# Kernel optimization log

Measured on AMD Instinct MI355X. Metric: run time of the kernel, lower is better.

The kernel has to match this reference:

```python
import jax, jax.numpy as jnp
import numpy as np

EPS = 1e-6
TEMP = 1.0
L = 64  # shapelet_len


def _znorm(a):
    # z-normalize over last axis, population std, clamped by EPS (matches torch unbiased=False + clamp_min)
    mean = a.mean(axis=-1, keepdims=True)
    std = jnp.maximum(a.std(axis=-1, keepdims=True), EPS)
    return (a - mean) / std


def setup_inputs() -> dict:
    key = jax.random.key(0)
    k1, k2 = jax.random.split(key)
    bs, T, C, P = 32, 8192, 1, 64
    x = jax.random.normal(k1, (bs, T, C), dtype=jnp.float32)
    shapelets = jax.random.normal(k2, (P, C, L), dtype=jnp.float32)
    return {"x": x, "shapelets": shapelets}


def reference(x, shapelets):
    # x: [bs, T, C]; shapelets: [P, C, L]
    bs, T, C = x.shape
    P = shapelets.shape[0]
    x_ct = jnp.transpose(x, (0, 2, 1))  # [bs, C, T]
    Tp = T - L + 1
    # sliding windows: [bs, C, T', L]
    idx = jnp.arange(Tp)[:, None] + jnp.arange(L)[None, :]
    w = x_ct[:, :, idx]
    # z-normalize windows and shapelets over the length axis
    w = _znorm(w)
    s = _znorm(shapelets)
    # squared euclidean distance via expansion ||w||^2 - 2 w.s + ||s||^2 (sum over C and L)
    w2 = jnp.sum(w * w, axis=(1, 3))          # [bs, T']
    s2 = jnp.sum(s * s, axis=(1, 2))          # [P]
    dot = jnp.einsum('bctl,pcl->btp', w, s)   # [bs, T', P]
    dist2 = w2[:, :, None] + s2[None, None, :] - 2.0 * dot
    temp = max(TEMP, EPS)
    act = jnp.exp(-dist2 / temp)              # [bs, T', P]
    # center-pad to length T: left = L//2, right = T - (T' + left)
    left = L // 2
    right = max(0, T - (Tp + left))
    act_full = jnp.pad(act, ((0, 0), (left, right), (0, 0)))
    return act_full[:, :T, :]
```

## Files before the change

### kernel.cpp

```cpp
#include <hip/hip_runtime.h>
#include <math.h>

#define T_LEN 8192
#define EPSF  1e-6f

typedef __attribute__((ext_vector_type(8))) short short8;
typedef __attribute__((ext_vector_type(4))) float float4v;


__global__ __launch_bounds__(64, 1) void shapelet_prep(
        const float* __restrict__ sh, void* __restrict__ ws) {
    unsigned short* Bhi_g = (unsigned short*)ws;
    unsigned short* Blo_g = Bhi_g + 64 * 64;
    float* lsum_g = (float*)((char*)ws + 16384);
    float* ls2_g  = lsum_g + 64;

    const int p = threadIdx.x;
    const int c = ((p & 3) << 4) + (p >> 2);

    float S[64];
    const float4* s4 = (const float4*)(sh + (size_t)p * 64);
#pragma unroll
    for (int i = 0; i < 16; ++i) {
        float4 v = s4[i];
        S[4 * i + 0] = v.x;
        S[4 * i + 1] = v.y;
        S[4 * i + 2] = v.z;
        S[4 * i + 3] = v.w;
    }

    float s1 = 0.f;
#pragma unroll
    for (int l = 0; l < 64; ++l) s1 += S[l];
    float mu = s1 * (1.f / 64.f);
    float sq = 0.f;
#pragma unroll
    for (int l = 0; l < 64; ++l) { float d = S[l] - mu; sq = fmaf(d, d, sq); }
    float sd  = fmaxf(sqrtf(sq * (1.f / 64.f)), EPSF);
    float inv = 1.f / sd;
    float ssum = 0.f, ss2 = 0.f;
#pragma unroll
    for (int l2 = 0; l2 < 32; ++l2) {
        unsigned pk_h, pk_l;
        {
            float v = S[2 * l2];
            float s = (v - mu) * inv;
            unsigned ub = __float_as_uint(s);
            float hi = __uint_as_float(ub & 0xFFFF0000u);
            float lo = s - hi;
            unsigned lb = __float_as_uint(lo) & 0xFFFF0000u;
            pk_h = ub >> 16;
            pk_l = lb >> 16;
            float eff = hi + __uint_as_float(lb);
            ssum += eff;
            ss2  = fmaf(eff, eff, ss2);
        }
        {
            float v = S[2 * l2 + 1];
            float s = (v - mu) * inv;
            unsigned ub = __float_as_uint(s);
            float hi = __uint_as_float(ub & 0xFFFF0000u);
            float lo = s - hi;
            unsigned lb = __float_as_uint(lo) & 0xFFFF0000u;
            pk_h |= (ub & 0xFFFF0000u);
            pk_l |= lb;
            float eff = hi + __uint_as_float(lb);
            ssum += eff;
            ss2  = fmaf(eff, eff, ss2);
        }
        *(unsigned*)&Bhi_g[c * 64 + 2 * l2] = pk_h;
        *(unsigned*)&Blo_g[c * 64 + 2 * l2] = pk_l;
    }
    lsum_g[p] = ssum;
    ls2_g[p]  = ss2;
}

__global__ __launch_bounds__(256, 4) void shapelet_main(
        const float* __restrict__ x,
        const void* __restrict__ ws,
        float* __restrict__ out) {
    __shared__ __align__(16) float xs[320];
    __shared__ float4 lstat[256];

    const int tid  = threadIdx.x;
    const int lane = tid & 63;
    const int wave = tid >> 6;
    const int n    = lane & 15;
    const int quad = lane >> 4;

    const int super = blockIdx.x & 31;
    const int b     = blockIdx.x >> 5;
    const int t0    = super << 8;

    const unsigned short* Bhi_g = (const unsigned short*)ws;
    const unsigned short* Blo_g = Bhi_g + 64 * 64;
    const float* lsum_g = (const float*)((const char*)ws + 16384);

    short8 Bh[4][2], Bl[4][2];
#pragma unroll
    for (int pt = 0; pt < 4; ++pt)
#pragma unroll
        for (int h = 0; h < 2; ++h) {
            int off = ((pt * 16 + n) << 6) + (h << 5) + (quad << 3);
            Bh[pt][h] = *(const short8*)(Bhi_g + off);
            Bl[pt][h] = *(const short8*)(Blo_g + off);
        }
    const float4 sm4 = *(const float4*)(lsum_g + (n << 2));
    const float4 sv4 = *(const float4*)(lsum_g + 64 + (n << 2));

    if (tid < 80) {
        int g0 = t0 - 32 + (tid << 2);
        float4 v;
        if (g0 >= 0 && g0 + 3 < T_LEN) {
            v = *(const float4*)(x + (size_t)b * T_LEN + g0);
        } else {
            float* vp = (float*)&v;
#pragma unroll
            for (int e = 0; e < 4; ++e) {
                int g = g0 + e;
                vp[e] = ((unsigned)g < (unsigned)T_LEN) ? x[(size_t)b * T_LEN + g] : 0.f;
            }
        }
        *(float4*)&xs[tid << 2] = v;
    }
    __syncthreads();

    {
        const int r = tid;
        float s1 = 0.f, sq = 0.f;
#pragma unroll
        for (int l = 0; l < 64; ++l) {
            float v = xs[r + l];
            s1 += v; sq = fmaf(v, v, sq);
        }
        float mu  = s1 * (1.f / 64.f);
        float var = fmaxf(sq * (1.f / 64.f) - mu * mu, 0.f);
        float sd  = fmaxf(sqrtf(var), EPSF);
        float inv = 1.f / sd;
        float4 st;
        st.x = mu;
        st.y = inv;
        st.z = 64.f * var * inv * inv;
        st.w = 0.f;
        lstat[r] = st;
    }
    __syncthreads();

#pragma unroll
    for (int u = 0; u < 4; ++u) {
        const int abase = (u << 6) + (wave << 4) + n + (quad << 3);
        short8 Ah[2], Al[2];
#pragma unroll
        for (int h = 0; h < 2; ++h) {
#pragma unroll
            for (int j = 0; j < 8; ++j) {
                float v = xs[abase + h * 32 + j];
                unsigned ub = __float_as_uint(v);
                unsigned hb = ub & 0xFFFF0000u;
                float lo = v - __uint_as_float(hb);
                Ah[h][j] = (short)(ub >> 16);
                Al[h][j] = (short)(__float_as_uint(lo) >> 16);
            }
        }

        float4v acc[4];
#pragma unroll
        for (int pt = 0; pt < 4; ++pt) {
            float4v a = {0.f, 0.f, 0.f, 0.f};
#pragma unroll
            for (int h = 0; h < 2; ++h) {
                a = __builtin_amdgcn_mfma_f32_16x16x32_bf16(Ah[h], Bh[pt][h], a, 0, 0, 0);
                a = __builtin_amdgcn_mfma_f32_16x16x32_bf16(Ah[h], Bl[pt][h], a, 0, 0, 0);
                a = __builtin_amdgcn_mfma_f32_16x16x32_bf16(Al[h], Bh[pt][h], a, 0, 0, 0);
            }
            acc[pt] = a;
        }

#pragma unroll
        for (int r = 0; r < 4; ++r) {
            int tl = (u << 6) + (wave << 4) + (quad << 2) + r;
            int tg = t0 + tl;
            bool valid = (tg >= 32) && (tg <= 8160);
            float4 st = lstat[tl];
            float mu  = st.x;
            float inv = st.y;
            float w2  = st.z;
            float d0 = (acc[0][r] - mu * sm4.x) * inv;
            float d1 = (acc[1][r] - mu * sm4.y) * inv;
            float d2 = (acc[2][r] - mu * sm4.z) * inv;
            float d3 = (acc[3][r] - mu * sm4.w) * inv;
            float4 o;
            o.x = valid ? __expf(-(w2 + sv4.x - 2.f * d0)) : 0.f;
            o.y = valid ? __expf(-(w2 + sv4.y - 2.f * d1)) : 0.f;
            o.z = valid ? __expf(-(w2 + sv4.z - 2.f * d2)) : 0.f;
            o.w = valid ? __expf(-(w2 + sv4.w - 2.f * d3)) : 0.f;
            *(float4*)(out + (((size_t)(b * T_LEN + tg)) << 6) + (n << 2)) = o;
        }
    }
}

extern "C" void kernel_launch(void* const* d_in, const int* in_sizes, int n_in,
                              void* d_out, int out_size, void* d_ws, size_t ws_size,
                              hipStream_t stream) {
    const float* x  = (const float*)d_in[0];
    const float* sh = (const float*)d_in[1];
    float* out = (float*)d_out;

    shapelet_prep<<<1, 64, 0, stream>>>(sh, d_ws);
    shapelet_main<<<32 * 32, 256, 0, stream>>>(x, d_ws, out);
}
```

Baseline: 87.24 us.

## Fuse shapelet preprocessing into main kernel via shared memory

Removes the separate single-block prep kernel and has every block's first wave normalize and split the shapelets into bf16 hi/lo parts in LDS, while other threads load the x tile. This eliminates one kernel launch and the serial dependency on a tiny prep kernel. In exchange every one of the 1024 blocks redoes the shapelet normalization (64 threads × 64 elements) and uses more LDS, which may reduce occupancy.

```diff
diff --git a/kernel.cpp b/kernel.cpp
--- a/kernel.cpp
+++ b/kernel.cpp
@@ -7,80 +7,16 @@
 typedef __attribute__((ext_vector_type(8))) short short8;
 typedef __attribute__((ext_vector_type(4))) float float4v;
 
-
-__global__ __launch_bounds__(64, 1) void shapelet_prep(
-        const float* __restrict__ sh, void* __restrict__ ws) {
-    unsigned short* Bhi_g = (unsigned short*)ws;
-    unsigned short* Blo_g = Bhi_g + 64 * 64;
-    float* lsum_g = (float*)((char*)ws + 16384);
-    float* ls2_g  = lsum_g + 64;
-
-    const int p = threadIdx.x;
-    const int c = ((p & 3) << 4) + (p >> 2);
-
-    float S[64];
-    const float4* s4 = (const float4*)(sh + (size_t)p * 64);
-#pragma unroll
-    for (int i = 0; i < 16; ++i) {
-        float4 v = s4[i];
-        S[4 * i + 0] = v.x;
-        S[4 * i + 1] = v.y;
-        S[4 * i + 2] = v.z;
-        S[4 * i + 3] = v.w;
-    }
-
-    float s1 = 0.f;
-#pragma unroll
-    for (int l = 0; l < 64; ++l) s1 += S[l];
-    float mu = s1 * (1.f / 64.f);
-    float sq = 0.f;
-#pragma unroll
-    for (int l = 0; l < 64; ++l) { float d = S[l] - mu; sq = fmaf(d, d, sq); }
-    float sd  = fmaxf(sqrtf(sq * (1.f / 64.f)), EPSF);
-    float inv = 1.f / sd;
-    float ssum = 0.f, ss2 = 0.f;
-#pragma unroll
-    for (int l2 = 0; l2 < 32; ++l2) {
-        unsigned pk_h, pk_l;
-        {
-            float v = S[2 * l2];
-            float s = (v - mu) * inv;
-            unsigned ub = __float_as_uint(s);
-            float hi = __uint_as_float(ub & 0xFFFF0000u);
-            float lo = s - hi;
-            unsigned lb = __float_as_uint(lo) & 0xFFFF0000u;
-            pk_h = ub >> 16;
-            pk_l = lb >> 16;
-            float eff = hi + __uint_as_float(lb);
-            ssum += eff;
-            ss2  = fmaf(eff, eff, ss2);
-        }
-        {
-            float v = S[2 * l2 + 1];
-            float s = (v - mu) * inv;
-            unsigned ub = __float_as_uint(s);
-            float hi = __uint_as_float(ub & 0xFFFF0000u);
-            float lo = s - hi;
-            unsigned lb = __float_as_uint(lo) & 0xFFFF0000u;
-            pk_h |= (ub & 0xFFFF0000u);
-            pk_l |= lb;
-            float eff = hi + __uint_as_float(lb);
-            ssum += eff;
-            ss2  = fmaf(eff, eff, ss2);
-        }
-        *(unsigned*)&Bhi_g[c * 64 + 2 * l2] = pk_h;
-        *(unsigned*)&Blo_g[c * 64 + 2 * l2] = pk_l;
-    }
-    lsum_g[p] = ssum;
-    ls2_g[p]  = ss2;
-}
-
-__global__ __launch_bounds__(256, 4) void shapelet_main(
+__global__ __launch_bounds__(256, 4) void shapelet_fused(
         const float* __restrict__ x,
-        const void* __restrict__ ws,
+        const float* __restrict__ sh,
         float* __restrict__ out) {
+    __shared__ unsigned short Bhi[64][72];
+    __shared__ unsigned short Blo[64][72];
     __shared__ __align__(16) float xs[320];
     __shared__ float4 lstat[256];
+    __shared__ __align__(16) float lsum[64];
+    __shared__ __align__(16) float ls2[64];
 
     const int tid  = threadIdx.x;
     const int lane = tid & 63;
@@ -92,24 +28,68 @@
     const int b     = blockIdx.x >> 5;
     const int t0    = super << 8;
 
-    const unsigned short* Bhi_g = (const unsigned short*)ws;
-    const unsigned short* Blo_g = Bhi_g + 64 * 64;
-    const float* lsum_g = (const float*)((const char*)ws + 16384);
-
-    short8 Bh[4][2], Bl[4][2];
-#pragma unroll
-    for (int pt = 0; pt < 4; ++pt)
-#pragma unroll
-        for (int h = 0; h < 2; ++h) {
-            int off = ((pt * 16 + n) << 6) + (h << 5) + (quad << 3);
-            Bh[pt][h] = *(const short8*)(Bhi_g + off);
-            Bl[pt][h] = *(const short8*)(Blo_g + off);
-        }
-    const float4 sm4 = *(const float4*)(lsum_g + (n << 2));
-    const float4 sv4 = *(const float4*)(lsum_g + 64 + (n << 2));
-
-    if (tid < 80) {
-        int g0 = t0 - 32 + (tid << 2);
+    if (tid < 64) {
+        const int p = tid;
+        const int c = ((p & 3) << 4) + (p >> 2);
+
+        float S[64];
+        const float4* s4 = (const float4*)(sh + (size_t)p * 64);
+#pragma unroll
+        for (int i = 0; i < 16; ++i) {
+            float4 v = s4[i];
+            S[4 * i + 0] = v.x;
+            S[4 * i + 1] = v.y;
+            S[4 * i + 2] = v.z;
+            S[4 * i + 3] = v.w;
+        }
+
+        float s1 = 0.f;
+#pragma unroll
+        for (int l = 0; l < 64; ++l) s1 += S[l];
+        float mu = s1 * (1.f / 64.f);
+        float sq = 0.f;
+#pragma unroll
+        for (int l = 0; l < 64; ++l) { float d = S[l] - mu; sq = fmaf(d, d, sq); }
+        float sd  = fmaxf(sqrtf(sq * (1.f / 64.f)), EPSF);
+        float inv = 1.f / sd;
+        float ssum = 0.f, ss2 = 0.f;
+#pragma unroll
+        for (int l2 = 0; l2 < 32; ++l2) {
+            unsigned pk_h, pk_l;
+            {
+                float v = S[2 * l2];
+                float s = (v - mu) * inv;
+                unsigned ub = __float_as_uint(s);
+                float hi = __uint_as_float(ub & 0xFFFF0000u);
+                float lo = s - hi;
+                unsigned lb = __float_as_uint(lo) & 0xFFFF0000u;
+                pk_h = ub >> 16;
+                pk_l = lb >> 16;
+                float eff = hi + __uint_as_float(lb);
+                ssum += eff;
+                ss2  = fmaf(eff, eff, ss2);
+            }
+            {
+                float v = S[2 * l2 + 1];
+                float s = (v - mu) * inv;
+                unsigned ub = __float_as_uint(s);
+                float hi = __uint_as_float(ub & 0xFFFF0000u);
+                float lo = s - hi;
+                unsigned lb = __float_as_uint(lo) & 0xFFFF0000u;
+                pk_h |= (ub & 0xFFFF0000u);
+                pk_l |= lb;
+                float eff = hi + __uint_as_float(lb);
+                ssum += eff;
+                ss2  = fmaf(eff, eff, ss2);
+            }
+            *(unsigned*)&Bhi[c][2 * l2] = pk_h;
+            *(unsigned*)&Blo[c][2 * l2] = pk_l;
+        }
+        lsum[p] = ssum;
+        ls2[p]  = ss2;
+    } else if (tid < 144) {
+        const int i = tid - 64;
+        int g0 = t0 - 32 + (i << 2);
         float4 v;
         if (g0 >= 0 && g0 + 3 < T_LEN) {
             v = *(const float4*)(x + (size_t)b * T_LEN + g0);
@@ -121,7 +101,7 @@
                 vp[e] = ((unsigned)g < (unsigned)T_LEN) ? x[(size_t)b * T_LEN + g] : 0.f;
             }
         }
-        *(float4*)&xs[tid << 2] = v;
+        *(float4*)&xs[i << 2] = v;
     }
     __syncthreads();
 
@@ -144,6 +124,17 @@
         st.w = 0.f;
         lstat[r] = st;
     }
+
+    short8 Bh[4][2], Bl[4][2];
+#pragma unroll
+    for (int pt = 0; pt < 4; ++pt)
+#pragma unroll
+        for (int h = 0; h < 2; ++h) {
+            Bh[pt][h] = *(const short8*)&Bhi[pt * 16 + n][h * 32 + (quad << 3)];
+            Bl[pt][h] = *(const short8*)&Blo[pt * 16 + n][h * 32 + (quad << 3)];
+        }
+    const float4 sm4 = *(const float4*)&lsum[n << 2];
+    const float4 sv4 = *(const float4*)&ls2[n << 2];
     __syncthreads();
 
 #pragma unroll
@@ -206,6 +197,5 @@
     const float* sh = (const float*)d_in[1];
     float* out = (float*)d_out;
 
-    shapelet_prep<<<1, 64, 0, stream>>>(sh, d_ws);
-    shapelet_main<<<32 * 32, 256, 0, stream>>>(x, d_ws, out);
+    shapelet_fused<<<32 * 32, 256, 0, stream>>>(x, sh, out);
 }
```

New measurement: 83.33 us. 4.5% less time.
